# Kernel tuning notes

Measured on AMD Instinct MI355X. Metric: run time of the kernel, lower is better.

The kernel has to match this reference:

```python
import jax, jax.numpy as jnp
import numpy as np

# -------- configuration (production-scale segmentation head) --------
BS, C, H, W = 8, 256, 96, 96
N = H * W          # nodes in the spanning tree (flattened pixels)
E = N - 1          # spanning-tree edge count
ZETA_G = 0.01      # default zeta_g of Global_APro.forward


def setup_inputs() -> dict:
    key = jax.random.key(0)
    k1, k2 = jax.random.split(key)
    feature_in = jax.random.normal(k1, (BS, 1, H, W), dtype=jnp.float32)
    # scaled so norm2 distances over C=256 channels stay O(1..10)
    embed_in = 0.1 * jax.random.normal(k2, (BS, C, H, W), dtype=jnp.float32)
    # Random spanning trees, one per batch element. Edges are topologically
    # ordered: edge e connects parent=src[e] < child=tgt[e]=e+1, so processing
    # edges in order is a valid root->leaf sweep (and reversed is leaf->root).
    rng = np.random.default_rng(0)
    trees = []
    children = np.arange(1, N, dtype=np.int32)
    for _ in range(BS):
        parents = np.floor(rng.random(E) * np.arange(1, N)).astype(np.int32)
        trees.append(np.stack([parents, children], axis=1))
    tree = jnp.asarray(np.stack(trees, axis=0))  # [BS, E, 2] int32
    return {"feature_in": feature_in, "embed_in": embed_in, "tree": tree}


def _gp_single(f, wgt, src, tgt):
    """Global affinity propagation (tree filter) on one tree.
    Computes out_i = sum_j A_ij f_j / sum_j A_ij with A_ij = prod of edge
    affinities along the unique tree path i->j, via the classic two-pass DP.
    f: [N], wgt/src/tgt: [E] (edges topologically ordered, parent=src).
    """
    ones = jnp.ones_like(f)

    def up(carry, xs):                 # leaf -> root aggregation
        S, Z = carry
        s, t, we = xs
        S = S.at[s].add(we * S[t])
        Z = Z.at[s].add(we * Z[t])
        return (S, Z), None

    (S, Z), _ = jax.lax.scan(up, (f, ones), (src, tgt, wgt), reverse=True)

    def down(carry, xs):               # root -> leaf propagation
        F, G = carry
        s, t, we = xs
        F = F.at[t].set(we * F[s] + (1.0 - we * we) * F[t])
        G = G.at[t].set(we * G[s] + (1.0 - we * we) * G[t])
        return (F, G), None

    (F, G), _ = jax.lax.scan(down, (S, Z), (src, tgt, wgt))
    return F / G


def reference(feature_in, embed_in, tree):
    bs, c, h, w = embed_in.shape
    n = h * w
    emb = embed_in.reshape(bs, c, n)               # [bs, c, N]
    src = tree[:, :, 0]                            # [bs, E]
    tgt = tree[:, :, 1]                            # [bs, E]
    # gather node embeddings along tree edges (get_true_index)
    gather = jax.vmap(lambda e, i: e[:, i])        # [c, N], [E] -> [c, E]
    src_node = gather(emb, src)                    # [bs, c, E]
    tgt_node = gather(emb, tgt)                    # [bs, c, E]
    diff = src_node - tgt_node
    dist = jnp.sum(diff * diff, axis=1)            # norm2_distance -> [bs, E]
    wgt = jnp.exp(-ZETA_G * dist)                  # edge affinity
    f = feature_in.reshape(bs, n)                  # [bs, N]
    out = jax.vmap(_gp_single)(f, wgt, src, tgt)   # [bs, N]
    return out.reshape(bs, 1, h, w)
```

## Files before the change

### kernel.cpp

```cpp
#include <hip/hip_runtime.h>
#include <hip/hip_bf16.h>
#include <hip/hip_fp16.h>

#define BS 8
#define C  256
#define N  9216
#define E  9215
#define MAXD 128
#define LVL_STRIDE 192
#define TSLABS (N / 64)

__global__ __launch_bounds__(1024) void setup_kernel(const float* __restrict__ emb,
                                                     __half* __restrict__ embT,
                                                     const int* __restrict__ tree,
                                                     int* __restrict__ tsArr,
                                                     int* __restrict__ lvlOff) {
    __shared__ int P[N];
    __shared__ int cnt[MAXD];
    __shared__ int off[MAXD + 1];
    const int tid = threadIdx.x;

    if (blockIdx.x < BS) {
        const int b = blockIdx.x;
        const int* tb = tree + b * E * 2;

        for (int t = tid; t < N; t += 1024)
            P[t] = (t == 0) ? 0 : (tb[(t - 1) * 2] | (1 << 16));
        for (int i = tid; i < MAXD; i += 1024) cnt[i] = 0;
        __syncthreads();

        for (int it = 0; it < 6; ++it) {
            int np[9];
            int k = 0;
            for (int t = tid; t < N; t += 1024, ++k) {
                int p = P[t];
                int pa = P[p & 0xffff];
                np[k] = (pa & 0xffff) | ((p >> 16) + (pa >> 16)) << 16;
            }
            __syncthreads();
            k = 0;
            for (int t = tid; t < N; t += 1024, ++k) P[t] = np[k];
            __syncthreads();
        }

        for (int t = 1 + tid; t < N; t += 1024) {
            int d = P[t] >> 16; if (d > MAXD - 1) d = MAXD - 1;
            atomicAdd(&cnt[d], 1);
        }
        __syncthreads();
        if (tid == 0) {
            int acc = 0, mx = 1;
            for (int d = 0; d < MAXD; ++d) {
                off[d] = acc; acc += cnt[d];
                if (cnt[d] > 0) mx = d;
            }
            off[MAXD] = acc;
            lvlOff[b * LVL_STRIDE + MAXD + 1] = mx;
        }
        __syncthreads();
        for (int i = tid; i < MAXD; i += 1024) cnt[i] = 0;
        __syncthreads();

        for (int t = 1 + tid; t < N; t += 1024) {
            int d = P[t] >> 16; if (d > MAXD - 1) d = MAXD - 1;
            int pos = off[d] + atomicAdd(&cnt[d], 1);
            int p = tb[(t - 1) * 2];
            tsArr[b * N + pos] = t | (p << 16);
        }
        for (int i = tid; i <= MAXD; i += 1024) lvlOff[b * LVL_STRIDE + i] = off[i];
    } else {
        const int tb = blockIdx.x - BS;
        const int b  = tb & 7;
        const int n0 = (tb >> 3) * 64;
        __half (*tile)[65] = (__half(*)[65])P;

        const int nn = tid & 63;
        const int cg = tid >> 6;
        const float* src = emb + (size_t)b * C * N + n0;
        #pragma unroll
        for (int k = 0; k < 16; ++k) {
            int cc = cg * 16 + k;
            tile[cc][nn] = __float2half(src[(size_t)cc * N + nn]);
        }
        __syncthreads();

        const int cp = tid & 127;
        const int ng = tid >> 7;
        __half* dst = embT + ((size_t)b * N + n0) * C;
        #pragma unroll
        for (int k = 0; k < 8; ++k) {
            int n2 = ng * 8 + k;
            __half2 v = __halves2half2(tile[2 * cp][n2], tile[2 * cp + 1][n2]);
            *(__half2*)(dst + (size_t)n2 * C + 2 * cp) = v;
        }
    }
}

__global__ __launch_bounds__(256) void weights_kernel(const __half* __restrict__ embT,
                                                      const int* __restrict__ tree,
                                                      float* __restrict__ wgt) {
    const int b   = blockIdx.y;
    const int tid = threadIdx.x;
    const int lane = tid & 63;
    const int wid  = tid >> 6;
    const int sub  = lane >> 5;
    const int l    = lane & 31;
    const int e    = (blockIdx.x * 4 + wid) * 2 + sub;

    float acc = 0.f;
    if (e < E) {
        int s = tree[(b * E + e) * 2];
        int t = tree[(b * E + e) * 2 + 1];
        const float4* ps = (const float4*)(embT + ((size_t)b * N + s) * C) + l;
        const float4* pt = (const float4*)(embT + ((size_t)b * N + t) * C) + l;
        float4 av = *ps;
        float4 bv = *pt;
        const __half2* ah = (const __half2*)&av;
        const __half2* bh = (const __half2*)&bv;
        #pragma unroll
        for (int j = 0; j < 4; ++j) {
            float2 fa = __half22float2(ah[j]);
            float2 fb = __half22float2(bh[j]);
            float d0 = fa.x - fb.x;
            float d1 = fa.y - fb.y;
            acc += d0 * d0 + d1 * d1;
        }
    }
    #pragma unroll
    for (int m = 16; m >= 1; m >>= 1) acc += __shfl_xor(acc, m);
    if (l == 0 && e < E) wgt[b * N + e] = __expf(-0.01f * acc);
}

__global__ __launch_bounds__(1024) void dp_kernel(const float* __restrict__ feat,
                                                  const int* __restrict__ lvlOff,
                                                  const int* __restrict__ tsArr,
                                                  const float* __restrict__ wgt,
                                                  float* __restrict__ out) {
    const int b = blockIdx.x;
    const int tid = threadIdx.x;
    __shared__ float2 V[N];
    __shared__ int2 TSW[N];
    __shared__ int off[MAXD + 1];
    __shared__ int maxd_s;

    for (int i = tid; i <= MAXD; i += 1024) off[i] = lvlOff[b * LVL_STRIDE + i];
    if (tid == 0) maxd_s = lvlOff[b * LVL_STRIDE + MAXD + 1];

    const int* tsA = tsArr + b * N;
    const float* wG = wgt + b * N;
    for (int i = tid; i < N; i += 1024)
        V[i] = make_float2(feat[b * N + i], 1.0f);
    for (int i = tid; i < E; i += 1024) {
        int ts = tsA[i];
        float w = wG[(ts & 0xffff) - 1];
        TSW[i] = make_int2(ts, __float_as_int(w));
    }
    __syncthreads();
    const int maxd = maxd_s;

    for (int lev = maxd; lev >= 1; --lev) {
        int s0 = off[lev], s1 = off[lev + 1];
        for (int i = s0 + tid; i < s1; i += 1024) {
            int2 ew = TSW[i];
            int t = ew.x & 0xffff, s = ew.x >> 16;
            float w = __int_as_float(ew.y);
            float2 vt = V[t];
            atomicAdd(&V[s].x, w * vt.x);
            atomicAdd(&V[s].y, w * vt.y);
        }
        __syncthreads();
    }
    for (int lev = 1; lev <= maxd; ++lev) {
        int s0 = off[lev], s1 = off[lev + 1];
        for (int i = s0 + tid; i < s1; i += 1024) {
            int2 ew = TSW[i];
            int t = ew.x & 0xffff, s = ew.x >> 16;
            float w = __int_as_float(ew.y);
            float2 vs = V[s], vt = V[t];
            float c = 1.f - w * w;
            V[t] = make_float2(w * vs.x + c * vt.x, w * vs.y + c * vt.y);
        }
        __syncthreads();
    }
    for (int i = tid; i < N; i += 1024) {
        float2 v = V[i];
        out[b * N + i] = v.x / v.y;
    }
}

extern "C" void kernel_launch(void* const* d_in, const int* in_sizes, int n_in,
                              void* d_out, int out_size, void* d_ws, size_t ws_size,
                              hipStream_t stream) {
    const float* feat = (const float*)d_in[0];
    const float* emb  = (const float*)d_in[1];
    const int*   tree = (const int*)d_in[2];
    float* out = (float*)d_out;

    const size_t BN = (size_t)BS * N;
    float* wgt    = (float*)d_ws;
    int*   tsArr  = (int*)((char*)d_ws + BN * 4);
    int*   lvlOff = (int*)((char*)d_ws + BN * 8);
    __half* embT  = (__half*)((char*)d_ws +
                     ((BN * 8 + BS * LVL_STRIDE * 4 + 255) / 256) * 256);

    setup_kernel<<<BS + TSLABS * BS, 1024, 0, stream>>>(emb, embT, tree, tsArr, lvlOff);
    weights_kernel<<<dim3((E + 7) / 8, BS), 256, 0, stream>>>(embT, tree, wgt);
    dp_kernel<<<BS, 1024, 0, stream>>>(feat, lvlOff, tsArr, wgt, out);
}
```

Baseline: 175.7 us.

## Group up-sweep edges by parent to pair children and avoid atomics

Reorders each level's edge list so siblings sharing a parent sit contiguously, and records per-slot flags (pair length, many-children flag). In the up-sweep, one thread now combines up to two children before writing to the parent, and uses a plain read-modify-write when the parent has at most two children, keeping atomics only for high-fanout parents. This aims to cut shared-memory atomic traffic in the serial per-level DP, at the cost of extra setup work (child counts, a second scatter pass) and an extra byte array loaded into LDS.

```diff
diff --git a/kernel.cpp b/kernel.cpp
--- a/kernel.cpp
+++ b/kernel.cpp
@@ -13,9 +13,11 @@
 __global__ __launch_bounds__(1024) void setup_kernel(const float* __restrict__ emb,
                                                      __half* __restrict__ embT,
                                                      const int* __restrict__ tree,
-                                                     int* __restrict__ tsArr,
+                                                     int* __restrict__ uparr,
+                                                     unsigned char* __restrict__ lenG,
                                                      int* __restrict__ lvlOff) {
     __shared__ int P[N];
+    __shared__ unsigned int CC[N];
     __shared__ int cnt[MAXD];
     __shared__ int off[MAXD + 1];
     const int tid = threadIdx.x;
@@ -24,8 +26,10 @@
         const int b = blockIdx.x;
         const int* tb = tree + b * E * 2;
 
-        for (int t = tid; t < N; t += 1024)
+        for (int t = tid; t < N; t += 1024) {
             P[t] = (t == 0) ? 0 : (tb[(t - 1) * 2] | (1 << 16));
+            CC[t] = 0u;
+        }
         for (int i = tid; i < MAXD; i += 1024) cnt[i] = 0;
         __syncthreads();
 
@@ -46,6 +50,8 @@
         for (int t = 1 + tid; t < N; t += 1024) {
             int d = P[t] >> 16; if (d > MAXD - 1) d = MAXD - 1;
             atomicAdd(&cnt[d], 1);
+            int p = tb[(t - 1) * 2];
+            atomicAdd(&CC[p], 1u);
         }
         __syncthreads();
         if (tid == 0) {
@@ -61,11 +67,35 @@
         for (int i = tid; i < MAXD; i += 1024) cnt[i] = 0;
         __syncthreads();
 
+        for (int p = tid; p < N; p += 1024) {
+            unsigned int c = CC[p];
+            if (c > 0) {
+                int dlev = (P[p] >> 16) + 1; if (dlev > MAXD - 1) dlev = MAXD - 1;
+                int base = off[dlev] + atomicAdd(&cnt[dlev], (int)c);
+                P[p] = (P[p] & 0xffff0000) | base;
+            }
+        }
+        for (int i = tid; i < N; i += 1024) lenG[b * N + i] = 0;
+        __syncthreads();
+
+        for (int p = tid; p < N; p += 1024) {
+            unsigned int c = CC[p];
+            if (c > 0) {
+                int base = P[p] & 0xffff;
+                unsigned char fl = (c > 2u) ? 4 : 0;
+                for (unsigned int j = 0; j < c; j += 2) {
+                    unsigned char ln = (j + 2 <= c) ? 2 : 1;
+                    lenG[b * N + base + j] = ln | fl;
+                }
+            }
+        }
+        __syncthreads();
+
         for (int t = 1 + tid; t < N; t += 1024) {
-            int d = P[t] >> 16; if (d > MAXD - 1) d = MAXD - 1;
-            int pos = off[d] + atomicAdd(&cnt[d], 1);
             int p = tb[(t - 1) * 2];
-            tsArr[b * N + pos] = t | (p << 16);
+            unsigned int o = atomicSub(&CC[p], 1u) - 1u;
+            int slot = (P[p] & 0xffff) + (int)o;
+            uparr[b * N + slot] = t | (p << 16);
         }
         for (int i = tid; i <= MAXD; i += 1024) lvlOff[b * LVL_STRIDE + i] = off[i];
     } else {
@@ -133,23 +163,28 @@
 
 __global__ __launch_bounds__(1024) void dp_kernel(const float* __restrict__ feat,
                                                   const int* __restrict__ lvlOff,
-                                                  const int* __restrict__ tsArr,
+                                                  const int* __restrict__ uparr,
+                                                  const unsigned char* __restrict__ lenG,
                                                   const float* __restrict__ wgt,
                                                   float* __restrict__ out) {
     const int b = blockIdx.x;
     const int tid = threadIdx.x;
     __shared__ float2 V[N];
     __shared__ int2 TSW[N];
+    __shared__ unsigned char LEN[N];
     __shared__ int off[MAXD + 1];
     __shared__ int maxd_s;
 
     for (int i = tid; i <= MAXD; i += 1024) off[i] = lvlOff[b * LVL_STRIDE + i];
     if (tid == 0) maxd_s = lvlOff[b * LVL_STRIDE + MAXD + 1];
 
-    const int* tsA = tsArr + b * N;
+    const int* tsA = uparr + b * N;
     const float* wG = wgt + b * N;
-    for (int i = tid; i < N; i += 1024)
+    const unsigned char* lG = lenG + b * N;
+    for (int i = tid; i < N; i += 1024) {
         V[i] = make_float2(feat[b * N + i], 1.0f);
+        LEN[i] = lG[i];
+    }
     for (int i = tid; i < E; i += 1024) {
         int ts = tsA[i];
         float w = wG[(ts & 0xffff) - 1];
@@ -158,21 +193,39 @@
     __syncthreads();
     const int maxd = maxd_s;
 
+    int s1 = off[maxd + 1];
     for (int lev = maxd; lev >= 1; --lev) {
-        int s0 = off[lev], s1 = off[lev + 1];
+        int s0 = off[lev];
         for (int i = s0 + tid; i < s1; i += 1024) {
-            int2 ew = TSW[i];
-            int t = ew.x & 0xffff, s = ew.x >> 16;
-            float w = __int_as_float(ew.y);
-            float2 vt = V[t];
-            atomicAdd(&V[s].x, w * vt.x);
-            atomicAdd(&V[s].y, w * vt.y);
-        }
-        __syncthreads();
-    }
+            int lb = LEN[i];
+            if (lb) {
+                int2 e0 = TSW[i];
+                int p = e0.x >> 16;
+                float w0 = __int_as_float(e0.y);
+                float2 v0 = V[e0.x & 0xffff];
+                float ax = w0 * v0.x, ay = w0 * v0.y;
+                if (lb & 2) {
+                    int2 e1 = TSW[i + 1];
+                    float w1 = __int_as_float(e1.y);
+                    float2 v1 = V[e1.x & 0xffff];
+                    ax += w1 * v1.x; ay += w1 * v1.y;
+                }
+                if (lb & 4) {
+                    atomicAdd(&V[p].x, ax);
+                    atomicAdd(&V[p].y, ay);
+                } else {
+                    float2 vp = V[p];
+                    V[p] = make_float2(vp.x + ax, vp.y + ay);
+                }
+            }
+        }
+        s1 = s0;
+        __syncthreads();
+    }
+    int s0 = off[1];
     for (int lev = 1; lev <= maxd; ++lev) {
-        int s0 = off[lev], s1 = off[lev + 1];
-        for (int i = s0 + tid; i < s1; i += 1024) {
+        int s1d = off[lev + 1];
+        for (int i = s0 + tid; i < s1d; i += 1024) {
             int2 ew = TSW[i];
             int t = ew.x & 0xffff, s = ew.x >> 16;
             float w = __int_as_float(ew.y);
@@ -180,6 +233,7 @@
             float c = 1.f - w * w;
             V[t] = make_float2(w * vs.x + c * vt.x, w * vs.y + c * vt.y);
         }
+        s0 = s1d;
         __syncthreads();
     }
     for (int i = tid; i < N; i += 1024) {
@@ -198,12 +252,13 @@
 
     const size_t BN = (size_t)BS * N;
     float* wgt    = (float*)d_ws;
-    int*   tsArr  = (int*)((char*)d_ws + BN * 4);
+    int*   uparr  = (int*)((char*)d_ws + BN * 4);
     int*   lvlOff = (int*)((char*)d_ws + BN * 8);
+    unsigned char* lenG = (unsigned char*)((char*)d_ws + BN * 8 + BS * LVL_STRIDE * 4);
     __half* embT  = (__half*)((char*)d_ws +
-                     ((BN * 8 + BS * LVL_STRIDE * 4 + 255) / 256) * 256);
-
-    setup_kernel<<<BS + TSLABS * BS, 1024, 0, stream>>>(emb, embT, tree, tsArr, lvlOff);
+                     ((BN * 9 + BS * LVL_STRIDE * 4 + 255) / 256) * 256);
+
+    setup_kernel<<<BS + TSLABS * BS, 1024, 0, stream>>>(emb, embT, tree, uparr, lenG, lvlOff);
     weights_kernel<<<dim3((E + 7) / 8, BS), 256, 0, stream>>>(embT, tree, wgt);
-    dp_kernel<<<BS, 1024, 0, stream>>>(feat, lvlOff, tsArr, wgt, out);
-}
+    dp_kernel<<<BS, 1024, 0, stream>>>(feat, lvlOff, uparr, lenG, wgt, out);
+}
```

New measurement: 171.4 us. -2.5%, faster.

## Shrink DP block to 128 threads, prefetch level edges, scatter weights into slot order

Applied to the files above, without the earlier changes.

The tree DP kernel now runs with 128 threads per block, so the per-level barriers are cheaper, and it prefetches the next level's first edge before each barrier. The setup kernel's pointer jumping now alternates between two buffers and stops at root ancestors. Level counting uses 8-way split counters and a parallel prefix scan in place of a serial loop, and it records each edge's slot. The weights kernel scatters each weight straight into the slot-ordered edge array, which removes the indirect gather in the DP. The costs are fewer threads for wide levels, an extra slot array, and scattered 4-byte writes to global memory.

```diff
diff --git a/kernel.cpp b/kernel.cpp
--- a/kernel.cpp
+++ b/kernel.cpp
@@ -13,62 +13,20 @@
 __global__ __launch_bounds__(1024) void setup_kernel(const float* __restrict__ emb,
                                                      __half* __restrict__ embT,
                                                      const int* __restrict__ tree,
-                                                     int* __restrict__ tsArr,
+                                                     int2* __restrict__ tswG,
+                                                     int* __restrict__ slotG,
                                                      int* __restrict__ lvlOff) {
     __shared__ int P[N];
-    __shared__ int cnt[MAXD];
+    __shared__ int U[N];
+    __shared__ int SLOT[N];
+    __shared__ int cnt8[MAXD * 8];
+    __shared__ int tot[MAXD];
+    __shared__ int sc1[MAXD];
     __shared__ int off[MAXD + 1];
+    __shared__ int maxd_sh;
     const int tid = threadIdx.x;
 
-    if (blockIdx.x < BS) {
-        const int b = blockIdx.x;
-        const int* tb = tree + b * E * 2;
-
-        for (int t = tid; t < N; t += 1024)
-            P[t] = (t == 0) ? 0 : (tb[(t - 1) * 2] | (1 << 16));
-        for (int i = tid; i < MAXD; i += 1024) cnt[i] = 0;
-        __syncthreads();
-
-        for (int it = 0; it < 6; ++it) {
-            int np[9];
-            int k = 0;
-            for (int t = tid; t < N; t += 1024, ++k) {
-                int p = P[t];
-                int pa = P[p & 0xffff];
-                np[k] = (pa & 0xffff) | ((p >> 16) + (pa >> 16)) << 16;
-            }
-            __syncthreads();
-            k = 0;
-            for (int t = tid; t < N; t += 1024, ++k) P[t] = np[k];
-            __syncthreads();
-        }
-
-        for (int t = 1 + tid; t < N; t += 1024) {
-            int d = P[t] >> 16; if (d > MAXD - 1) d = MAXD - 1;
-            atomicAdd(&cnt[d], 1);
-        }
-        __syncthreads();
-        if (tid == 0) {
-            int acc = 0, mx = 1;
-            for (int d = 0; d < MAXD; ++d) {
-                off[d] = acc; acc += cnt[d];
-                if (cnt[d] > 0) mx = d;
-            }
-            off[MAXD] = acc;
-            lvlOff[b * LVL_STRIDE + MAXD + 1] = mx;
-        }
-        __syncthreads();
-        for (int i = tid; i < MAXD; i += 1024) cnt[i] = 0;
-        __syncthreads();
-
-        for (int t = 1 + tid; t < N; t += 1024) {
-            int d = P[t] >> 16; if (d > MAXD - 1) d = MAXD - 1;
-            int pos = off[d] + atomicAdd(&cnt[d], 1);
-            int p = tb[(t - 1) * 2];
-            tsArr[b * N + pos] = t | (p << 16);
-        }
-        for (int i = tid; i <= MAXD; i += 1024) lvlOff[b * LVL_STRIDE + i] = off[i];
-    } else {
+    if (blockIdx.x >= BS) {
         const int tb = blockIdx.x - BS;
         const int b  = tb & 7;
         const int n0 = (tb >> 3) * 64;
@@ -93,12 +51,95 @@
             __half2 v = __halves2half2(tile[2 * cp][n2], tile[2 * cp + 1][n2]);
             *(__half2*)(dst + (size_t)n2 * C + 2 * cp) = v;
         }
-    }
+        return;
+    }
+
+    const int b = blockIdx.x;
+    const int* tb = tree + b * E * 2;
+
+    for (int t = tid; t < N; t += 1024)
+        P[t] = (t == 0) ? 0 : (tb[(t - 1) * 2] | (1 << 16));
+    for (int i = tid; i < MAXD * 8; i += 1024) cnt8[i] = 0;
+    if (tid == 0) maxd_sh = 1;
+    __syncthreads();
+
+    for (int r = 0; r < 3; ++r) {
+        for (int t = tid; t < N; t += 1024) {
+            int p = P[t];
+            int a = p & 0xffff;
+            if (a == 0) U[t] = p;
+            else {
+                int pa = P[a];
+                U[t] = (pa & 0xffff) | (((p >> 16) + (pa >> 16)) << 16);
+            }
+        }
+        __syncthreads();
+        for (int t = tid; t < N; t += 1024) {
+            int p = U[t];
+            int a = p & 0xffff;
+            if (a == 0) P[t] = p;
+            else {
+                int pa = U[a];
+                P[t] = (pa & 0xffff) | (((p >> 16) + (pa >> 16)) << 16);
+            }
+        }
+        __syncthreads();
+    }
+
+    for (int t = 1 + tid; t < N; t += 1024) {
+        int d = P[t] >> 16;
+        atomicAdd(&cnt8[d * 8 + (tid >> 7)], 1);
+    }
+    __syncthreads();
+
+    for (int d = tid; d < MAXD; d += 1024) {
+        int s = 0;
+        #pragma unroll
+        for (int k = 0; k < 8; ++k) {
+            int v = cnt8[d * 8 + k];
+            cnt8[d * 8 + k] = s;
+            s += v;
+        }
+        tot[d] = s;
+        if (s > 0) atomicMax(&maxd_sh, d);
+    }
+    __syncthreads();
+
+    {
+        int* src = tot; int* dst = sc1;
+        for (int step = 1; step < MAXD; step <<= 1) {
+            for (int d = tid; d < MAXD; d += 1024)
+                dst[d] = src[d] + ((d >= step) ? src[d - step] : 0);
+            __syncthreads();
+            int* tmp = src; src = dst; dst = tmp;
+        }
+        for (int d = tid; d < MAXD; d += 1024) off[d + 1] = src[d];
+        if (tid == 0) off[0] = 0;
+    }
+    __syncthreads();
+
+    for (int t = 1 + tid; t < N; t += 1024) {
+        int d = P[t] >> 16;
+        int idx = atomicAdd(&cnt8[d * 8 + (tid >> 7)], 1);
+        int slot = off[d] + idx;
+        int p = tb[(t - 1) * 2];
+        U[slot] = t | (p << 16);
+        SLOT[t - 1] = slot;
+    }
+    __syncthreads();
+
+    for (int i = tid; i < E; i += 1024) {
+        tswG[b * N + i] = make_int2(U[i], 0);
+        slotG[b * N + i] = SLOT[i];
+    }
+    for (int i = tid; i <= MAXD; i += 1024) lvlOff[b * LVL_STRIDE + i] = off[i];
+    if (tid == 0) lvlOff[b * LVL_STRIDE + 129] = maxd_sh;
 }
 
 __global__ __launch_bounds__(256) void weights_kernel(const __half* __restrict__ embT,
                                                       const int* __restrict__ tree,
-                                                      float* __restrict__ wgt) {
+                                                      const int* __restrict__ slotG,
+                                                      int2* __restrict__ tswG) {
     const int b   = blockIdx.y;
     const int tid = threadIdx.x;
     const int lane = tid & 63;
@@ -110,7 +151,7 @@
     float acc = 0.f;
     if (e < E) {
         int s = tree[(b * E + e) * 2];
-        int t = tree[(b * E + e) * 2 + 1];
+        int t = e + 1;
         const float4* ps = (const float4*)(embT + ((size_t)b * N + s) * C) + l;
         const float4* pt = (const float4*)(embT + ((size_t)b * N + t) * C) + l;
         float4 av = *ps;
@@ -128,14 +169,16 @@
     }
     #pragma unroll
     for (int m = 16; m >= 1; m >>= 1) acc += __shfl_xor(acc, m);
-    if (l == 0 && e < E) wgt[b * N + e] = __expf(-0.01f * acc);
-}
-
-__global__ __launch_bounds__(1024) void dp_kernel(const float* __restrict__ feat,
-                                                  const int* __restrict__ lvlOff,
-                                                  const int* __restrict__ tsArr,
-                                                  const float* __restrict__ wgt,
-                                                  float* __restrict__ out) {
+    if (l == 0 && e < E) {
+        int slot = slotG[b * N + e];
+        tswG[b * N + slot].y = __float_as_int(__expf(-0.01f * acc));
+    }
+}
+
+__global__ __launch_bounds__(128) void dp_kernel(const float* __restrict__ feat,
+                                                 const int* __restrict__ lvlOff,
+                                                 const int2* __restrict__ tswG,
+                                                 float* __restrict__ out) {
     const int b = blockIdx.x;
     const int tid = threadIdx.x;
     __shared__ float2 V[N];
@@ -143,46 +186,76 @@
     __shared__ int off[MAXD + 1];
     __shared__ int maxd_s;
 
-    for (int i = tid; i <= MAXD; i += 1024) off[i] = lvlOff[b * LVL_STRIDE + i];
-    if (tid == 0) maxd_s = lvlOff[b * LVL_STRIDE + MAXD + 1];
-
-    const int* tsA = tsArr + b * N;
-    const float* wG = wgt + b * N;
-    for (int i = tid; i < N; i += 1024)
+    for (int i = tid; i <= MAXD; i += 128) off[i] = lvlOff[b * LVL_STRIDE + i];
+    if (tid == 0) maxd_s = lvlOff[b * LVL_STRIDE + 129];
+
+    const int2* tG = tswG + b * N;
+    for (int i = tid; i < N; i += 128)
         V[i] = make_float2(feat[b * N + i], 1.0f);
-    for (int i = tid; i < E; i += 1024) {
-        int ts = tsA[i];
-        float w = wG[(ts & 0xffff) - 1];
-        TSW[i] = make_int2(ts, __float_as_int(w));
-    }
+    for (int i = tid; i < E; i += 128)
+        TSW[i] = tG[i];
     __syncthreads();
     const int maxd = maxd_s;
 
-    for (int lev = maxd; lev >= 1; --lev) {
-        int s0 = off[lev], s1 = off[lev + 1];
-        for (int i = s0 + tid; i < s1; i += 1024) {
-            int2 ew = TSW[i];
-            int t = ew.x & 0xffff, s = ew.x >> 16;
-            float w = __int_as_float(ew.y);
-            float2 vt = V[t];
-            atomicAdd(&V[s].x, w * vt.x);
-            atomicAdd(&V[s].y, w * vt.y);
-        }
-        __syncthreads();
-    }
-    for (int lev = 1; lev <= maxd; ++lev) {
-        int s0 = off[lev], s1 = off[lev + 1];
-        for (int i = s0 + tid; i < s1; i += 1024) {
-            int2 ew = TSW[i];
-            int t = ew.x & 0xffff, s = ew.x >> 16;
-            float w = __int_as_float(ew.y);
-            float2 vs = V[s], vt = V[t];
-            float c = 1.f - w * w;
-            V[t] = make_float2(w * vs.x + c * vt.x, w * vs.y + c * vt.y);
-        }
-        __syncthreads();
-    }
-    for (int i = tid; i < N; i += 1024) {
+    {
+        int s0 = off[maxd], s1 = off[maxd + 1];
+        bool vp = (s0 + tid) < s1;
+        int2 pre = TSW[vp ? s0 + tid : 0];
+        for (int lev = maxd; lev >= 1; --lev) {
+            int ns0 = (lev > 1) ? off[lev - 1] : 0;
+            int ns1 = s0;
+            if (vp) {
+                int t = pre.x & 0xffff, p = pre.x >> 16;
+                float w = __int_as_float(pre.y);
+                float2 vt = V[t];
+                atomicAdd(&V[p].x, w * vt.x);
+                atomicAdd(&V[p].y, w * vt.y);
+            }
+            for (int i = s0 + tid + 128; i < s1; i += 128) {
+                int2 ew = TSW[i];
+                int t = ew.x & 0xffff, p = ew.x >> 16;
+                float w = __int_as_float(ew.y);
+                float2 vt = V[t];
+                atomicAdd(&V[p].x, w * vt.x);
+                atomicAdd(&V[p].y, w * vt.y);
+            }
+            bool nvp = (lev > 1) && ((ns0 + tid) < ns1);
+            int2 npre = TSW[nvp ? ns0 + tid : 0];
+            __syncthreads();
+            pre = npre; vp = nvp; s1 = ns1; s0 = ns0;
+        }
+    }
+
+    {
+        int d0 = off[1], d1 = off[2];
+        bool vp = (d0 + tid) < d1;
+        int2 pre = TSW[vp ? d0 + tid : 0];
+        for (int lev = 1; lev <= maxd; ++lev) {
+            int nd0 = d1;
+            int nd1 = off[(lev + 2 <= MAXD) ? lev + 2 : MAXD];
+            if (vp) {
+                int t = pre.x & 0xffff, s = pre.x >> 16;
+                float w = __int_as_float(pre.y);
+                float2 vs = V[s], vt = V[t];
+                float c = 1.f - w * w;
+                V[t] = make_float2(w * vs.x + c * vt.x, w * vs.y + c * vt.y);
+            }
+            for (int i = d0 + tid + 128; i < d1; i += 128) {
+                int2 ew = TSW[i];
+                int t = ew.x & 0xffff, s = ew.x >> 16;
+                float w = __int_as_float(ew.y);
+                float2 vs = V[s], vt = V[t];
+                float c = 1.f - w * w;
+                V[t] = make_float2(w * vs.x + c * vt.x, w * vs.y + c * vt.y);
+            }
+            bool nvp = (lev < maxd) && ((nd0 + tid) < nd1);
+            int2 npre = TSW[nvp ? nd0 + tid : 0];
+            __syncthreads();
+            pre = npre; vp = nvp; d0 = nd0; d1 = nd1;
+        }
+    }
+
+    for (int i = tid; i < N; i += 128) {
         float2 v = V[i];
         out[b * N + i] = v.x / v.y;
     }
@@ -197,13 +270,13 @@
     float* out = (float*)d_out;
 
     const size_t BN = (size_t)BS * N;
-    float* wgt    = (float*)d_ws;
-    int*   tsArr  = (int*)((char*)d_ws + BN * 4);
-    int*   lvlOff = (int*)((char*)d_ws + BN * 8);
-    __half* embT  = (__half*)((char*)d_ws +
-                     ((BN * 8 + BS * LVL_STRIDE * 4 + 255) / 256) * 256);
-
-    setup_kernel<<<BS + TSLABS * BS, 1024, 0, stream>>>(emb, embT, tree, tsArr, lvlOff);
-    weights_kernel<<<dim3((E + 7) / 8, BS), 256, 0, stream>>>(embT, tree, wgt);
-    dp_kernel<<<BS, 1024, 0, stream>>>(feat, lvlOff, tsArr, wgt, out);
-}
+    int2* tswG   = (int2*)d_ws;
+    int*  slotG  = (int*)((char*)d_ws + BN * 8);
+    int*  lvlOff = (int*)((char*)d_ws + BN * 12);
+    __half* embT = (__half*)((char*)d_ws +
+                    ((BN * 12 + BS * LVL_STRIDE * 4 + 255) / 256) * 256);
+
+    setup_kernel<<<BS + TSLABS * BS, 1024, 0, stream>>>(emb, embT, tree, tswG, slotG, lvlOff);
+    weights_kernel<<<dim3((E + 7) / 8, BS), 256, 0, stream>>>(embT, tree, slotG, tswG);
+    dp_kernel<<<BS, 128, 0, stream>>>(feat, lvlOff, tswG, out);
+}
```

New measurement: 202.2 us. +15.1%, slower.
